# Optimization experiments

Hardware: AMD Instinct MI355X
Metric: run time of the kernel (lower is better)

The kernel has to match this reference:

```python
import jax, jax.numpy as jnp
import numpy as np

NUM_HEADS = 16
EMBED = 1024


def setup_inputs() -> dict:
    key = jax.random.key(0)
    k1, k2, k3 = jax.random.split(key, 3)
    B, T, L = 2, 2048, EMBED
    x = jax.random.normal(k1, (B, T, L), dtype=jnp.float32)
    # Dense kernels (use_bias=False), scaled like lecun init
    W_attn = jax.random.normal(k2, (L, 3 * L), dtype=jnp.float32) / np.sqrt(L)
    W_proj = jax.random.normal(k3, (L, L), dtype=jnp.float32) / np.sqrt(L)
    return {"x": x, "W_attn": W_attn, "W_proj": W_proj}


def reference(x, W_attn, W_proj):
    B, T, L = x.shape
    H = NUM_HEADS
    Dh = L // H
    qkv = x @ W_attn                       # [B, T, 3L]
    q, k, v = jnp.split(qkv, 3, axis=2)
    # [B, T, L] -> [B, H, T, Dh]
    q = q.reshape(B, T, H, Dh).transpose(0, 2, 1, 3)
    k = k.reshape(B, T, H, Dh).transpose(0, 2, 1, 3)
    v = v.reshape(B, T, H, Dh).transpose(0, 2, 1, 3)
    # NOTE: faithful to the source, scale is rsqrt(full embedding size L), not head dim
    att = jnp.einsum('bhqd,bhkd->bhqk', q, k) * jax.lax.rsqrt(jnp.float32(L))
    causal = jnp.tril(jnp.ones((T, T), dtype=bool))[None, None]
    att = jnp.where(causal, att, float('-inf'))
    att = jax.nn.softmax(att, axis=-1)
    y = jnp.einsum('bhqk,bhkd->bhqd', att, v)      # [B, H, T, Dh]
    y = y.transpose(0, 2, 1, 3).reshape(B, T, L)
    return y @ W_proj
```

## Files before the change

### kernel.cpp

```cpp
#include <hip/hip_runtime.h>
#include <math.h>

typedef unsigned short u16;
typedef unsigned int u32;
typedef short short8 __attribute__((ext_vector_type(8)));
typedef float f32x4 __attribute__((ext_vector_type(4)));
typedef float f4 __attribute__((ext_vector_type(4)));
typedef unsigned short u16x4 __attribute__((ext_vector_type(4)));
typedef unsigned int u32x2 __attribute__((ext_vector_type(2)));

__device__ __forceinline__ u16 f2bf(float f) {
  unsigned u = __builtin_bit_cast(unsigned, f);
  u += 0x7fffu + ((u >> 16) & 1u);
  return (u16)(u >> 16);
}

__device__ __forceinline__ float bf2f(u16 v) {
  return __builtin_bit_cast(float, (u32)v << 16);
}

__device__ __forceinline__ u32 cvtpk_bf16(float a, float b) {
  u32 r;
  asm("v_cvt_pk_bf16_f32 %0, %1, %2" : "=v"(r) : "v"(a), "v"(b));
  return r;
}

__device__ __forceinline__ float exp2r(float x) {
  float r;
  asm("v_exp_f32 %0, %1" : "=v"(r) : "v"(x));
  return r;
}

__device__ __forceinline__ void gload16(const void* g, void* l) {
  __builtin_amdgcn_global_load_lds((const __attribute__((address_space(1))) void*)g,
                                   (__attribute__((address_space(3))) void*)l, 16, 0, 0);
}

__global__ __launch_bounds__(256) void prep_kernel(const float* __restrict__ x,
                                                   u16* __restrict__ xb,
                                                   const float* __restrict__ Wa,
                                                   u16* __restrict__ Wat,
                                                   const float* __restrict__ Wp,
                                                   u16* __restrict__ Wpt, float qscale) {
  __shared__ float t[32][33];
  const int bx = blockIdx.x, tid = threadIdx.x;
  if (bx < 1024) {
    const int n4 = 4194304 / 4;
    for (int i = bx * 256 + tid; i < n4; i += 1024 * 256) {
      f4 v = ((const f4*)x)[i];
      u16x4 o;
      o[0] = f2bf(v[0]); o[1] = f2bf(v[1]); o[2] = f2bf(v[2]); o[3] = f2bf(v[3]);
      ((u16x4*)xb)[i] = o;
    }
    return;
  }
  const float* in;
  u16* out;
  int R, C, j0, i0, qcols;
  if (bx < 4096) {
    int bid = bx - 1024;
    in = Wa; out = Wat; R = 1024; C = 3072; qcols = 1024;
    j0 = (bid % 96) * 32; i0 = (bid / 96) * 32;
  } else {
    int bid = bx - 4096;
    in = Wp; out = Wpt; R = 1024; C = 1024; qcols = 0;
    j0 = (bid % 32) * 32; i0 = (bid / 32) * 32;
  }
  const int tx = tid & 31, ty = tid >> 5;
#pragma unroll
  for (int k = 0; k < 4; ++k) t[ty + 8 * k][tx] = in[(size_t)(i0 + ty + 8 * k) * C + j0 + tx];
  __syncthreads();
#pragma unroll
  for (int k = 0; k < 4; ++k) {
    int orow = j0 + ty + 8 * k;
    float v = t[tx][ty + 8 * k];
    if (orow < qcols) v *= qscale;
    out[(size_t)orow * R + i0 + tx] = f2bf(v);
  }
}

template <int MODE>
__global__ __launch_bounds__(256) void gemm_kernel(const u16* __restrict__ A,
                                                   const u16* __restrict__ Bt,
                                                   void* __restrict__ Cv,
                                                   u16* __restrict__ Vt, int N, int K) {
  __shared__ __align__(16) u16 lA[128 * 64];
  __shared__ __align__(16) u16 lB[128 * 64];
  const int tid = threadIdx.x;
  const int w = tid >> 6, lane = tid & 63, lo = lane & 15, hi = lane >> 4;
  const int wm = w >> 1, wn = w & 1;
  const int m0 = blockIdx.y * 128, n0 = blockIdx.x * 128;
  f32x4 acc[4][4] = {};
  const int nkt = K >> 6;
  for (int kt = 0; kt < nkt; ++kt) {
    const int k0 = kt * 64;
#pragma unroll
    for (int c = 0; c < 4; ++c) {
      int flat = tid + c * 256;
      int r = flat >> 3, kc = flat & 7;
      int kcs = kc ^ (r & 7);
      gload16(A + (size_t)(m0 + r) * K + k0 + kcs * 8, (char*)lA + flat * 16);
      gload16(Bt + (size_t)(n0 + r) * K + k0 + kcs * 8, (char*)lB + flat * 16);
    }
    __syncthreads();
#pragma unroll
    for (int kk = 0; kk < 2; ++kk) {
      short8 af[4], bf[4];
#pragma unroll
      for (int mf = 0; mf < 4; ++mf) {
        int row = wm * 64 + mf * 16 + lo;
        int addr = (row * 128 + kk * 64 + hi * 16) ^ ((row & 7) << 4);
        af[mf] = *(const short8*)((const char*)lA + addr);
      }
#pragma unroll
      for (int nf = 0; nf < 4; ++nf) {
        int row = wn * 64 + nf * 16 + lo;
        int addr = (row * 128 + kk * 64 + hi * 16) ^ ((row & 7) << 4);
        bf[nf] = *(const short8*)((const char*)lB + addr);
      }
#pragma unroll
      for (int mf = 0; mf < 4; ++mf)
#pragma unroll
        for (int nf = 0; nf < 4; ++nf)
          acc[mf][nf] = __builtin_amdgcn_mfma_f32_16x16x32_bf16(af[mf], bf[nf], acc[mf][nf], 0, 0, 0);
    }
    __syncthreads();
  }
#pragma unroll
  for (int mf = 0; mf < 4; ++mf)
#pragma unroll
    for (int nf = 0; nf < 4; ++nf) {
      const int row0 = m0 + wm * 64 + mf * 16 + hi * 4;
      const int col = n0 + wn * 64 + nf * 16 + lo;
      if (MODE == 0) {
#pragma unroll
        for (int r = 0; r < 4; ++r)
          ((float*)Cv)[(size_t)(row0 + r) * N + col] = acc[mf][nf][r];
      } else {
        if (col < 2048) {
#pragma unroll
          for (int r = 0; r < 4; ++r)
            ((u16*)Cv)[(size_t)(row0 + r) * N + col] = f2bf(acc[mf][nf][r]);
        } else {
          const int dl = col - 2048;
          const int bh = (row0 >> 11) * 16 + (dl >> 6);
          const int d = dl & 63, t = row0 & 2047;
          u16x4 pk;
#pragma unroll
          for (int r = 0; r < 4; ++r) pk[r] = f2bf(acc[mf][nf][r]);
          *(u16x4*)&Vt[(size_t)bh * 131072 + d * 2048 + t] = pk;
        }
      }
    }
}

__global__ __launch_bounds__(256) void gemm_proj(const u16* __restrict__ A,
                                                 const u16* __restrict__ Bt,
                                                 float* __restrict__ C, int N, int K) {
  __shared__ __align__(16) u16 lA[128 * 64];
  __shared__ __align__(16) u16 lB[64 * 64];
  const int tid = threadIdx.x;
  const int w = tid >> 6, lane = tid & 63, lo = lane & 15, hi = lane >> 4;
  const int wm = w >> 1, wn = w & 1;
  const int m0 = blockIdx.y * 128, n0 = blockIdx.x * 64;
  f32x4 acc[4][2] = {};
  const int nkt = K >> 6;
  for (int kt = 0; kt < nkt; ++kt) {
    const int k0 = kt * 64;
#pragma unroll
    for (int c = 0; c < 4; ++c) {
      int flat = tid + c * 256;
      int r = flat >> 3, kc = flat & 7;
      int kcs = kc ^ (r & 7);
      gload16(A + (size_t)(m0 + r) * K + k0 + kcs * 8, (char*)lA + flat * 16);
    }
#pragma unroll
    for (int c = 0; c < 2; ++c) {
      int flat = tid + c * 256;
      int r = flat >> 3, kc = flat & 7;
      int kcs = kc ^ (r & 7);
      gload16(Bt + (size_t)(n0 + r) * K + k0 + kcs * 8, (char*)lB + flat * 16);
    }
    __syncthreads();
#pragma unroll
    for (int kk = 0; kk < 2; ++kk) {
      short8 af[4], bf[2];
#pragma unroll
      for (int mf = 0; mf < 4; ++mf) {
        int row = wm * 64 + mf * 16 + lo;
        int addr = (row * 128 + kk * 64 + hi * 16) ^ ((row & 7) << 4);
        af[mf] = *(const short8*)((const char*)lA + addr);
      }
#pragma unroll
      for (int nf = 0; nf < 2; ++nf) {
        int row = wn * 32 + nf * 16 + lo;
        int addr = (row * 128 + kk * 64 + hi * 16) ^ ((row & 7) << 4);
        bf[nf] = *(const short8*)((const char*)lB + addr);
      }
#pragma unroll
      for (int mf = 0; mf < 4; ++mf)
#pragma unroll
        for (int nf = 0; nf < 2; ++nf)
          acc[mf][nf] = __builtin_amdgcn_mfma_f32_16x16x32_bf16(af[mf], bf[nf], acc[mf][nf], 0, 0, 0);
    }
    __syncthreads();
  }
#pragma unroll
  for (int mf = 0; mf < 4; ++mf)
#pragma unroll
    for (int nf = 0; nf < 2; ++nf) {
      const int row0 = m0 + wm * 64 + mf * 16 + hi * 4;
      const int col = n0 + wn * 32 + nf * 16 + lo;
#pragma unroll
      for (int r = 0; r < 4; ++r)
        C[(size_t)(row0 + r) * N + col] = acc[mf][nf][r];
    }
}

__global__ __launch_bounds__(512) void attn_kernel(const u16* __restrict__ qkv,
                                                   const u16* __restrict__ Vt,
                                                   u16* __restrict__ yb) {
  __shared__ __align__(16) u16 lK[2][64 * 64];
  __shared__ __align__(16) u16 lV[2][64 * 64];
  __shared__ __align__(16) u16 pl[8][16][72];
  const int tid = threadIdx.x, w = tid >> 6, lane = tid & 63;
  const int lo = lane & 15, hi = lane >> 4;
  const int id = blockIdx.x;
  const int j = id >> 5;
  const int qb = (j < 8) ? (15 - 2 * j) : (2 * (j - 8));
  const int bh = id & 31, b = bh >> 4, h = bh & 15;
  const int q0b = qb * 128;
  const int wq0 = q0b + w * 16;

  const int sr = tid >> 3, skc = tid & 7;
  const int skcs = (skc ^ (sr & 7)) * 8;
  const int kSrc = (b * 2048 + sr) * 3072 + 1024 + h * 64 + skcs;
  const int vSrc = bh * 131072 + sr * 2048 + skcs;
  const int sdst = tid * 16;

  const int qbase = (b * 2048 + wq0 + lo) * 3072 + h * 64 + hi * 8;
  const short8 qf0 = *(const short8*)(qkv + qbase);
  const short8 qf1 = *(const short8*)(qkv + qbase + 32);

  short8 vones;
#pragma unroll
  for (int i = 0; i < 8; ++i) vones[i] = (short)0x3F80;

  f32x4 yacc[4] = {};
  f32x4 lacc = {};

  const int nt = 2 * qb + 2;
  gload16(qkv + kSrc, (char*)lK[0] + sdst);
  gload16(Vt + vSrc, (char*)lV[0] + sdst);
  asm volatile("s_waitcnt vmcnt(0)" ::: "memory");
  __syncthreads();

  int buf = 0;
#pragma unroll 1
  for (int it = 0; it < nt; ++it) {
    const int t0 = it * 64;
    if (it + 1 < nt) {
      gload16(qkv + (kSrc + (t0 + 64) * 3072), (char*)lK[buf ^ 1] + sdst);
      gload16(Vt + (vSrc + t0 + 64), (char*)lV[buf ^ 1] + sdst);
    }
    if (t0 <= wq0 + 15) {
      const char* lKb = (const char*)lK[buf];
      const char* lVb = (const char*)lV[buf];
      short8 kf[4][2];
#pragma unroll
      for (int n = 0; n < 4; ++n)
#pragma unroll
        for (int kk = 0; kk < 2; ++kk)
          kf[n][kk] = *(const short8*)(lKb + ((n * 16 + lo) * 128 + (((kk * 4 + hi) ^ (lo & 7)) * 16)));
      f32x4 st[4] = {};
#pragma unroll
      for (int n = 0; n < 4; ++n)
        st[n] = __builtin_amdgcn_mfma_f32_16x16x32_bf16(kf[n][0], qf0, st[n], 0, 0, 0);
#pragma unroll
      for (int n = 0; n < 4; ++n)
        st[n] = __builtin_amdgcn_mfma_f32_16x16x32_bf16(kf[n][1], qf1, st[n], 0, 0, 0);

      if (t0 + 63 > wq0) {
        const int q = wq0 + lo;
#pragma unroll
        for (int n = 0; n < 4; ++n)
#pragma unroll
          for (int r = 0; r < 4; ++r) {
            const int k = t0 + n * 16 + hi * 4 + r;
            st[n][r] = (k <= q) ? st[n][r] : -INFINITY;
          }
      }
#pragma unroll
      for (int n = 0; n < 4; ++n) {
        u32x2 pw;
        pw[0] = cvtpk_bf16(exp2r(st[n][0]), exp2r(st[n][1]));
        pw[1] = cvtpk_bf16(exp2r(st[n][2]), exp2r(st[n][3]));
        *(u32x2*)&pl[w][lo][n * 16 + hi * 4] = pw;
      }
      short8 pa0 = *(const short8*)&pl[w][lo][hi * 8];
      short8 pa1 = *(const short8*)&pl[w][lo][32 + hi * 8];
      short8 vf0[4], vf1[4];
#pragma unroll
      for (int nf = 0; nf < 4; ++nf) {
        vf0[nf] = *(const short8*)(lVb + ((nf * 16 + lo) * 128 + (((hi) ^ (lo & 7)) * 16)));
        vf1[nf] = *(const short8*)(lVb + ((nf * 16 + lo) * 128 + (((4 + hi) ^ (lo & 7)) * 16)));
      }
#pragma unroll
      for (int nf = 0; nf < 4; ++nf)
        yacc[nf] = __builtin_amdgcn_mfma_f32_16x16x32_bf16(pa0, vf0[nf], yacc[nf], 0, 0, 0);
      lacc = __builtin_amdgcn_mfma_f32_16x16x32_bf16(pa0, vones, lacc, 0, 0, 0);
#pragma unroll
      for (int nf = 0; nf < 4; ++nf)
        yacc[nf] = __builtin_amdgcn_mfma_f32_16x16x32_bf16(pa1, vf1[nf], yacc[nf], 0, 0, 0);
      lacc = __builtin_amdgcn_mfma_f32_16x16x32_bf16(pa1, vones, lacc, 0, 0, 0);
    }
    asm volatile("s_waitcnt vmcnt(0)" ::: "memory");
    __syncthreads();
    buf ^= 1;
  }

  f32x4 inv;
#pragma unroll
  for (int r = 0; r < 4; ++r) inv[r] = 1.f / lacc[r];
#pragma unroll
  for (int nf = 0; nf < 4; ++nf)
#pragma unroll
    for (int r = 0; r < 4; ++r)
      yb[(b * 2048 + wq0 + hi * 4 + r) * 1024 + h * 64 + nf * 16 + lo] =
          f2bf(yacc[nf][r] * inv[r]);
}

extern "C" void kernel_launch(void* const* d_in, const int* in_sizes, int n_in,
                              void* d_out, int out_size, void* d_ws, size_t ws_size,
                              hipStream_t stream) {
  const float* x = (const float*)d_in[0];
  const float* Wa = (const float*)d_in[1];
  const float* Wp = (const float*)d_in[2];
  char* ws = (char*)d_ws;
  u16* xb   = (u16*)(ws);
  u16* Wat  = (u16*)(ws + 8388608);
  u16* Wpt  = (u16*)(ws + 14680064);
  u16* qkvb = (u16*)(ws + 16777216);
  u16* Vt   = (u16*)(ws + 41943040);
  u16* yb   = (u16*)(ws + 50331648);

  const float CS = 0.03125f * 1.44269504088896f;
  prep_kernel<<<5120, 256, 0, stream>>>(x, xb, Wa, Wat, Wp, Wpt, CS);
  gemm_kernel<2><<<dim3(24, 32), 256, 0, stream>>>(xb, Wat, (void*)qkvb, Vt, 3072, 1024);
  attn_kernel<<<512, 512, 0, stream>>>(qkvb, Vt, yb);
  gemm_proj<<<dim3(16, 32), 256, 0, stream>>>(yb, Wpt, (float*)d_out, 1024, 1024);
}
```

Measured before the change: 102.8 us.

## Give each attention wave two 16-row query tiles, halve block size

The attention kernel now runs 256 threads per block, with each of the 4 waves handling 32 query rows as two 16-row M tiles instead of 16 rows. Each K and V fragment read from LDS is reused across both M tiles, so LDS traffic per MFMA drops. Each thread now issues two global-to-LDS copies per tile. The cost is more accumulator registers, coarser causal skipping per wave, and fewer waves per block to hide latency.

```diff
diff --git a/kernel.cpp b/kernel.cpp
--- a/kernel.cpp
+++ b/kernel.cpp
@@ -217,41 +217,51 @@
     }
 }
 
-__global__ __launch_bounds__(512) void attn_kernel(const u16* __restrict__ qkv,
+__global__ __launch_bounds__(256) void attn_kernel(const u16* __restrict__ qkv,
                                                    const u16* __restrict__ Vt,
                                                    u16* __restrict__ yb) {
   __shared__ __align__(16) u16 lK[2][64 * 64];
   __shared__ __align__(16) u16 lV[2][64 * 64];
-  __shared__ __align__(16) u16 pl[8][16][72];
+  __shared__ __align__(16) u16 pl[4][32][72];
   const int tid = threadIdx.x, w = tid >> 6, lane = tid & 63;
   const int lo = lane & 15, hi = lane >> 4;
   const int id = blockIdx.x;
   const int j = id >> 5;
   const int qb = (j < 8) ? (15 - 2 * j) : (2 * (j - 8));
   const int bh = id & 31, b = bh >> 4, h = bh & 15;
-  const int q0b = qb * 128;
-  const int wq0 = q0b + w * 16;
-
-  const int sr = tid >> 3, skc = tid & 7;
-  const int skcs = (skc ^ (sr & 7)) * 8;
-  const int kSrc = (b * 2048 + sr) * 3072 + 1024 + h * 64 + skcs;
-  const int vSrc = bh * 131072 + sr * 2048 + skcs;
-  const int sdst = tid * 16;
-
-  const int qbase = (b * 2048 + wq0 + lo) * 3072 + h * 64 + hi * 8;
-  const short8 qf0 = *(const short8*)(qkv + qbase);
-  const short8 qf1 = *(const short8*)(qkv + qbase + 32);
+  const int wq0 = qb * 128 + w * 32;
+
+  int kSrc[2], vSrc[2];
+#pragma unroll
+  for (int c = 0; c < 2; ++c) {
+    const int flat = tid + c * 256;
+    const int sr = flat >> 3, skc = flat & 7;
+    const int skcs = (skc ^ (sr & 7)) * 8;
+    kSrc[c] = (b * 2048 + sr) * 3072 + 1024 + h * 64 + skcs;
+    vSrc[c] = bh * 131072 + sr * 2048 + skcs;
+  }
+
+  short8 qf[2][2];
+#pragma unroll
+  for (int m = 0; m < 2; ++m) {
+    const int qbase = (b * 2048 + wq0 + m * 16 + lo) * 3072 + h * 64 + hi * 8;
+    qf[m][0] = *(const short8*)(qkv + qbase);
+    qf[m][1] = *(const short8*)(qkv + qbase + 32);
+  }
 
   short8 vones;
 #pragma unroll
   for (int i = 0; i < 8; ++i) vones[i] = (short)0x3F80;
 
-  f32x4 yacc[4] = {};
-  f32x4 lacc = {};
+  f32x4 yacc[2][4] = {};
+  f32x4 lacc[2] = {};
 
   const int nt = 2 * qb + 2;
-  gload16(qkv + kSrc, (char*)lK[0] + sdst);
-  gload16(Vt + vSrc, (char*)lV[0] + sdst);
+#pragma unroll
+  for (int c = 0; c < 2; ++c) {
+    gload16(qkv + kSrc[c], (char*)lK[0] + (tid + c * 256) * 16);
+    gload16(Vt + vSrc[c], (char*)lV[0] + (tid + c * 256) * 16);
+  }
   asm volatile("s_waitcnt vmcnt(0)" ::: "memory");
   __syncthreads();
 
@@ -260,45 +270,57 @@
   for (int it = 0; it < nt; ++it) {
     const int t0 = it * 64;
     if (it + 1 < nt) {
-      gload16(qkv + (kSrc + (t0 + 64) * 3072), (char*)lK[buf ^ 1] + sdst);
-      gload16(Vt + (vSrc + t0 + 64), (char*)lV[buf ^ 1] + sdst);
-    }
-    if (t0 <= wq0 + 15) {
+#pragma unroll
+      for (int c = 0; c < 2; ++c) {
+        gload16(qkv + (kSrc[c] + (t0 + 64) * 3072), (char*)lK[buf ^ 1] + (tid + c * 256) * 16);
+        gload16(Vt + (vSrc[c] + t0 + 64), (char*)lV[buf ^ 1] + (tid + c * 256) * 16);
+      }
+    }
+    if (t0 <= wq0 + 31) {
       const char* lKb = (const char*)lK[buf];
       const char* lVb = (const char*)lV[buf];
-      short8 kf[4][2];
-#pragma unroll
-      for (int n = 0; n < 4; ++n)
-#pragma unroll
-        for (int kk = 0; kk < 2; ++kk)
-          kf[n][kk] = *(const short8*)(lKb + ((n * 16 + lo) * 128 + (((kk * 4 + hi) ^ (lo & 7)) * 16)));
-      f32x4 st[4] = {};
-#pragma unroll
-      for (int n = 0; n < 4; ++n)
-        st[n] = __builtin_amdgcn_mfma_f32_16x16x32_bf16(kf[n][0], qf0, st[n], 0, 0, 0);
-#pragma unroll
-      for (int n = 0; n < 4; ++n)
-        st[n] = __builtin_amdgcn_mfma_f32_16x16x32_bf16(kf[n][1], qf1, st[n], 0, 0, 0);
+      f32x4 st[4][2] = {};
+#pragma unroll
+      for (int kk = 0; kk < 2; ++kk) {
+        short8 kf[4];
+#pragma unroll
+        for (int n = 0; n < 4; ++n)
+          kf[n] = *(const short8*)(lKb + ((n * 16 + lo) * 128 + (((kk * 4 + hi) ^ (lo & 7)) * 16)));
+#pragma unroll
+        for (int n = 0; n < 4; ++n)
+#pragma unroll
+          for (int m = 0; m < 2; ++m)
+            st[n][m] = __builtin_amdgcn_mfma_f32_16x16x32_bf16(kf[n], qf[m][kk], st[n][m], 0, 0, 0);
+      }
 
       if (t0 + 63 > wq0) {
-        const int q = wq0 + lo;
-#pragma unroll
-        for (int n = 0; n < 4; ++n)
-#pragma unroll
-          for (int r = 0; r < 4; ++r) {
-            const int k = t0 + n * 16 + hi * 4 + r;
-            st[n][r] = (k <= q) ? st[n][r] : -INFINITY;
-          }
-      }
-#pragma unroll
-      for (int n = 0; n < 4; ++n) {
-        u32x2 pw;
-        pw[0] = cvtpk_bf16(exp2r(st[n][0]), exp2r(st[n][1]));
-        pw[1] = cvtpk_bf16(exp2r(st[n][2]), exp2r(st[n][3]));
-        *(u32x2*)&pl[w][lo][n * 16 + hi * 4] = pw;
-      }
-      short8 pa0 = *(const short8*)&pl[w][lo][hi * 8];
-      short8 pa1 = *(const short8*)&pl[w][lo][32 + hi * 8];
+#pragma unroll
+        for (int m = 0; m < 2; ++m) {
+          const int q = wq0 + m * 16 + lo;
+#pragma unroll
+          for (int n = 0; n < 4; ++n)
+#pragma unroll
+            for (int r = 0; r < 4; ++r) {
+              const int k = t0 + n * 16 + hi * 4 + r;
+              st[n][m][r] = (k <= q) ? st[n][m][r] : -INFINITY;
+            }
+        }
+      }
+#pragma unroll
+      for (int m = 0; m < 2; ++m)
+#pragma unroll
+        for (int n = 0; n < 4; ++n) {
+          u32x2 pw;
+          pw[0] = cvtpk_bf16(exp2r(st[n][m][0]), exp2r(st[n][m][1]));
+          pw[1] = cvtpk_bf16(exp2r(st[n][m][2]), exp2r(st[n][m][3]));
+          *(u32x2*)&pl[w][m * 16 + lo][n * 16 + hi * 4] = pw;
+        }
+      short8 pa0[2], pa1[2];
+#pragma unroll
+      for (int m = 0; m < 2; ++m) {
+        pa0[m] = *(const short8*)&pl[w][m * 16 + lo][hi * 8];
+        pa1[m] = *(const short8*)&pl[w][m * 16 + lo][32 + hi * 8];
+      }
       short8 vf0[4], vf1[4];
 #pragma unroll
       for (int nf = 0; nf < 4; ++nf) {
@@ -306,28 +328,37 @@
         vf1[nf] = *(const short8*)(lVb + ((nf * 16 + lo) * 128 + (((4 + hi) ^ (lo & 7)) * 16)));
       }
 #pragma unroll
-      for (int nf = 0; nf < 4; ++nf)
-        yacc[nf] = __builtin_amdgcn_mfma_f32_16x16x32_bf16(pa0, vf0[nf], yacc[nf], 0, 0, 0);
-      lacc = __builtin_amdgcn_mfma_f32_16x16x32_bf16(pa0, vones, lacc, 0, 0, 0);
-#pragma unroll
-      for (int nf = 0; nf < 4; ++nf)
-        yacc[nf] = __builtin_amdgcn_mfma_f32_16x16x32_bf16(pa1, vf1[nf], yacc[nf], 0, 0, 0);
-      lacc = __builtin_amdgcn_mfma_f32_16x16x32_bf16(pa1, vones, lacc, 0, 0, 0);
+      for (int m = 0; m < 2; ++m) {
+#pragma unroll
+        for (int nf = 0; nf < 4; ++nf)
+          yacc[m][nf] = __builtin_amdgcn_mfma_f32_16x16x32_bf16(pa0[m], vf0[nf], yacc[m][nf], 0, 0, 0);
+        lacc[m] = __builtin_amdgcn_mfma_f32_16x16x32_bf16(pa0[m], vones, lacc[m], 0, 0, 0);
+      }
+#pragma unroll
+      for (int m = 0; m < 2; ++m) {
+#pragma unroll
+        for (int nf = 0; nf < 4; ++nf)
+          yacc[m][nf] = __builtin_amdgcn_mfma_f32_16x16x32_bf16(pa1[m], vf1[nf], yacc[m][nf], 0, 0, 0);
+        lacc[m] = __builtin_amdgcn_mfma_f32_16x16x32_bf16(pa1[m], vones, lacc[m], 0, 0, 0);
+      }
     }
     asm volatile("s_waitcnt vmcnt(0)" ::: "memory");
     __syncthreads();
     buf ^= 1;
   }
 
-  f32x4 inv;
-#pragma unroll
-  for (int r = 0; r < 4; ++r) inv[r] = 1.f / lacc[r];
-#pragma unroll
-  for (int nf = 0; nf < 4; ++nf)
-#pragma unroll
-    for (int r = 0; r < 4; ++r)
-      yb[(b * 2048 + wq0 + hi * 4 + r) * 1024 + h * 64 + nf * 16 + lo] =
-          f2bf(yacc[nf][r] * inv[r]);
+#pragma unroll
+  for (int m = 0; m < 2; ++m) {
+    f32x4 inv;
+#pragma unroll
+    for (int r = 0; r < 4; ++r) inv[r] = 1.f / lacc[m][r];
+#pragma unroll
+    for (int nf = 0; nf < 4; ++nf)
+#pragma unroll
+      for (int r = 0; r < 4; ++r)
+        yb[(b * 2048 + wq0 + m * 16 + hi * 4 + r) * 1024 + h * 64 + nf * 16 + lo] =
+            f2bf(yacc[m][nf][r] * inv[r]);
+  }
 }
 
 extern "C" void kernel_launch(void* const* d_in, const int* in_sizes, int n_in,
@@ -347,6 +378,6 @@
   const float CS = 0.03125f * 1.44269504088896f;
   prep_kernel<<<5120, 256, 0, stream>>>(x, xb, Wa, Wat, Wp, Wpt, CS);
   gemm_kernel<2><<<dim3(24, 32), 256, 0, stream>>>(xb, Wat, (void*)qkvb, Vt, 3072, 1024);
-  attn_kernel<<<512, 512, 0, stream>>>(qkvb, Vt, yb);
+  attn_kernel<<<512, 256, 0, stream>>>(qkvb, Vt, yb);
   gemm_proj<<<dim3(16, 32), 256, 0, stream>>>(yb, Wpt, (float*)d_out, 1024, 1024);
 }
```

Result: slower. 107.3 us (+4.3%).

## Keep attention P in registers and remap QKV GEMM blocks per XCD

Applied to the files above, without the earlier changes.

The attention kernel no longer writes exponentiated scores to a per-wave LDS scratch and reads them back. It packs the bf16 probabilities from the QK^T accumulators directly into MFMA A operands. The V fragments are gathered with a permuted key ordering so they match the accumulator register layout, at the cost of two 8-byte LDS reads per fragment instead of one 16-byte read. Separately, the QKV GEMM moves to a 1D grid with an XCD-aware block-to-tile mapping so that blocks on the same XCD share A/B tiles in L2.

```diff
diff --git a/kernel.cpp b/kernel.cpp
--- a/kernel.cpp
+++ b/kernel.cpp
@@ -4,19 +4,16 @@
 typedef unsigned short u16;
 typedef unsigned int u32;
 typedef short short8 __attribute__((ext_vector_type(8)));
+typedef short s16x4 __attribute__((ext_vector_type(4)));
 typedef float f32x4 __attribute__((ext_vector_type(4)));
 typedef float f4 __attribute__((ext_vector_type(4)));
 typedef unsigned short u16x4 __attribute__((ext_vector_type(4)));
-typedef unsigned int u32x2 __attribute__((ext_vector_type(2)));
+typedef unsigned int u32x4 __attribute__((ext_vector_type(4)));
 
 __device__ __forceinline__ u16 f2bf(float f) {
   unsigned u = __builtin_bit_cast(unsigned, f);
   u += 0x7fffu + ((u >> 16) & 1u);
   return (u16)(u >> 16);
-}
-
-__device__ __forceinline__ float bf2f(u16 v) {
-  return __builtin_bit_cast(float, (u32)v << 16);
 }
 
 __device__ __forceinline__ u32 cvtpk_bf16(float a, float b) {
@@ -79,17 +76,20 @@
   }
 }
 
-template <int MODE>
-__global__ __launch_bounds__(256) void gemm_kernel(const u16* __restrict__ A,
-                                                   const u16* __restrict__ Bt,
-                                                   void* __restrict__ Cv,
-                                                   u16* __restrict__ Vt, int N, int K) {
+__global__ __launch_bounds__(256) void gemm_qkv(const u16* __restrict__ A,
+                                                const u16* __restrict__ Bt,
+                                                u16* __restrict__ qkvb,
+                                                u16* __restrict__ Vt, int N, int K) {
   __shared__ __align__(16) u16 lA[128 * 64];
   __shared__ __align__(16) u16 lB[128 * 64];
   const int tid = threadIdx.x;
   const int w = tid >> 6, lane = tid & 63, lo = lane & 15, hi = lane >> 4;
   const int wm = w >> 1, wn = w & 1;
-  const int m0 = blockIdx.y * 128, n0 = blockIdx.x * 128;
+  const int id = blockIdx.x;
+  const int xcd = id & 7, kk0 = id >> 3;
+  const int py = kk0 & 7, px = kk0 >> 3;
+  const int m0 = (8 * (xcd >> 1) + py) * 128;
+  const int n0 = (12 * (xcd & 1) + px) * 128;
   f32x4 acc[4][4] = {};
   const int nkt = K >> 6;
   for (int kt = 0; kt < nkt; ++kt) {
@@ -132,24 +132,18 @@
     for (int nf = 0; nf < 4; ++nf) {
       const int row0 = m0 + wm * 64 + mf * 16 + hi * 4;
       const int col = n0 + wn * 64 + nf * 16 + lo;
-      if (MODE == 0) {
+      if (col < 2048) {
 #pragma unroll
         for (int r = 0; r < 4; ++r)
-          ((float*)Cv)[(size_t)(row0 + r) * N + col] = acc[mf][nf][r];
+          qkvb[(size_t)(row0 + r) * N + col] = f2bf(acc[mf][nf][r]);
       } else {
-        if (col < 2048) {
-#pragma unroll
-          for (int r = 0; r < 4; ++r)
-            ((u16*)Cv)[(size_t)(row0 + r) * N + col] = f2bf(acc[mf][nf][r]);
-        } else {
-          const int dl = col - 2048;
-          const int bh = (row0 >> 11) * 16 + (dl >> 6);
-          const int d = dl & 63, t = row0 & 2047;
-          u16x4 pk;
-#pragma unroll
-          for (int r = 0; r < 4; ++r) pk[r] = f2bf(acc[mf][nf][r]);
-          *(u16x4*)&Vt[(size_t)bh * 131072 + d * 2048 + t] = pk;
-        }
+        const int dl = col - 2048;
+        const int bh = (row0 >> 11) * 16 + (dl >> 6);
+        const int d = dl & 63, t = row0 & 2047;
+        u16x4 pk;
+#pragma unroll
+        for (int r = 0; r < 4; ++r) pk[r] = f2bf(acc[mf][nf][r]);
+        *(u16x4*)&Vt[(size_t)bh * 131072 + d * 2048 + t] = pk;
       }
     }
 }
@@ -222,15 +216,13 @@
                                                    u16* __restrict__ yb) {
   __shared__ __align__(16) u16 lK[2][64 * 64];
   __shared__ __align__(16) u16 lV[2][64 * 64];
-  __shared__ __align__(16) u16 pl[8][16][72];
   const int tid = threadIdx.x, w = tid >> 6, lane = tid & 63;
   const int lo = lane & 15, hi = lane >> 4;
   const int id = blockIdx.x;
   const int j = id >> 5;
   const int qb = (j < 8) ? (15 - 2 * j) : (2 * (j - 8));
   const int bh = id & 31, b = bh >> 4, h = bh & 15;
-  const int q0b = qb * 128;
-  const int wq0 = q0b + w * 16;
+  const int wq0 = qb * 128 + w * 16;
 
   const int sr = tid >> 3, skc = tid & 7;
   const int skcs = (skc ^ (sr & 7)) * 8;
@@ -290,29 +282,39 @@
             st[n][r] = (k <= q) ? st[n][r] : -INFINITY;
           }
       }
-#pragma unroll
-      for (int n = 0; n < 4; ++n) {
-        u32x2 pw;
-        pw[0] = cvtpk_bf16(exp2r(st[n][0]), exp2r(st[n][1]));
-        pw[1] = cvtpk_bf16(exp2r(st[n][2]), exp2r(st[n][3]));
-        *(u32x2*)&pl[w][lo][n * 16 + hi * 4] = pw;
-      }
-      short8 pa0 = *(const short8*)&pl[w][lo][hi * 8];
-      short8 pa1 = *(const short8*)&pl[w][lo][32 + hi * 8];
-      short8 vf0[4], vf1[4];
-#pragma unroll
-      for (int nf = 0; nf < 4; ++nf) {
-        vf0[nf] = *(const short8*)(lVb + ((nf * 16 + lo) * 128 + (((hi) ^ (lo & 7)) * 16)));
-        vf1[nf] = *(const short8*)(lVb + ((nf * 16 + lo) * 128 + (((4 + hi) ^ (lo & 7)) * 16)));
-      }
-#pragma unroll
-      for (int nf = 0; nf < 4; ++nf)
-        yacc[nf] = __builtin_amdgcn_mfma_f32_16x16x32_bf16(pa0, vf0[nf], yacc[nf], 0, 0, 0);
-      lacc = __builtin_amdgcn_mfma_f32_16x16x32_bf16(pa0, vones, lacc, 0, 0, 0);
-#pragma unroll
-      for (int nf = 0; nf < 4; ++nf)
-        yacc[nf] = __builtin_amdgcn_mfma_f32_16x16x32_bf16(pa1, vf1[nf], yacc[nf], 0, 0, 0);
-      lacc = __builtin_amdgcn_mfma_f32_16x16x32_bf16(pa1, vones, lacc, 0, 0, 0);
+
+      u32x4 w0, w1;
+#pragma unroll
+      for (int n = 0; n < 2; ++n) {
+        w0[2 * n]     = cvtpk_bf16(exp2r(st[n][0]), exp2r(st[n][1]));
+        w0[2 * n + 1] = cvtpk_bf16(exp2r(st[n][2]), exp2r(st[n][3]));
+      }
+#pragma unroll
+      for (int n = 0; n < 2; ++n) {
+        w1[2 * n]     = cvtpk_bf16(exp2r(st[n + 2][0]), exp2r(st[n + 2][1]));
+        w1[2 * n + 1] = cvtpk_bf16(exp2r(st[n + 2][2]), exp2r(st[n + 2][3]));
+      }
+      const short8 pa0 = __builtin_bit_cast(short8, w0);
+      const short8 pa1 = __builtin_bit_cast(short8, w1);
+
+      const int cb0 = hi >> 1, boff = (hi & 1) * 8;
+#pragma unroll
+      for (int hh = 0; hh < 2; ++hh) {
+        const short8 pa = hh ? pa1 : pa0;
+        short8 vf[4];
+#pragma unroll
+        for (int nf = 0; nf < 4; ++nf) {
+          const char* rowp = lVb + (nf * 16 + lo) * 128;
+          const int sw = (lo & 7);
+          s16x4 va = *(const s16x4*)(rowp + (((hh * 4 + cb0) ^ sw) * 16) + boff);
+          s16x4 vb = *(const s16x4*)(rowp + (((hh * 4 + cb0 + 2) ^ sw) * 16) + boff);
+          vf[nf] = __builtin_shufflevector(va, vb, 0, 1, 2, 3, 4, 5, 6, 7);
+        }
+#pragma unroll
+        for (int nf = 0; nf < 4; ++nf)
+          yacc[nf] = __builtin_amdgcn_mfma_f32_16x16x32_bf16(pa, vf[nf], yacc[nf], 0, 0, 0);
+        lacc = __builtin_amdgcn_mfma_f32_16x16x32_bf16(pa, vones, lacc, 0, 0, 0);
+      }
     }
     asm volatile("s_waitcnt vmcnt(0)" ::: "memory");
     __syncthreads();
@@ -346,7 +348,7 @@
 
   const float CS = 0.03125f * 1.44269504088896f;
   prep_kernel<<<5120, 256, 0, stream>>>(x, xb, Wa, Wat, Wp, Wpt, CS);
-  gemm_kernel<2><<<dim3(24, 32), 256, 0, stream>>>(xb, Wat, (void*)qkvb, Vt, 3072, 1024);
+  gemm_qkv<<<768, 256, 0, stream>>>(xb, Wat, qkvb, Vt, 3072, 1024);
   attn_kernel<<<512, 512, 0, stream>>>(qkvb, Vt, yb);
   gemm_proj<<<dim3(16, 32), 256, 0, stream>>>(yb, Wpt, (float*)d_out, 1024, 1024);
 }
```

After: 105.0 us. 2.1% more time.
